# Performance work log

Hardware: AMD Instinct MI355X
Metric: run time of the kernel (lower is better)

Reference implementation:

```python
import jax, jax.numpy as jnp
import numpy as np

B, N, D = 8, 4096, 3
MAX_K = 16


def setup_inputs() -> dict:
    key = jax.random.key(0)
    k1, k2, k3 = jax.random.split(key, 3)
    x = jax.random.normal(k1, (B, N, D), dtype=jnp.float32)
    preds = jax.random.normal(k2, (B, N, D), dtype=jnp.float32)
    k_vector = jax.random.normal(k3, (MAX_K,), dtype=jnp.float32)  # learned param
    return {"x": x, "preds": preds, "k_vector": k_vector}


def _pairwise_dist(x):
    # Euclidean cdist via ||a||^2 + ||b||^2 - 2 a.b, avoiding a [B,N,N,D] tensor.
    sq = jnp.sum(x * x, axis=-1)                      # [B, N]
    inner = jnp.einsum('bnd,bmd->bnm', x, x)          # [B, N, N]
    d2 = sq[:, :, None] + sq[:, None, :] - 2.0 * inner
    return jnp.sqrt(jnp.maximum(d2, 0.0))             # [B, N, N]


def reference(x, preds, k_vector):
    # k = argmax(softmax(k_vector)) + 1 ; softmax is monotone so argmax suffices.
    # In the torch original .item() makes k a Python int (static w.r.t. the graph).
    k = int(np.asarray(jnp.argmax(k_vector))) + 1

    dist = _pairwise_dist(x)                          # [B, N, N]
    # torch.topk(..., largest=False): k smallest distances -> top_k of negated.
    _, idx = jax.lax.top_k(-dist, k)                  # idx: [B, N, k]

    # Gather predicted coords of the k nearest neighbors per point.
    b_idx = jnp.arange(preds.shape[0])[:, None, None]  # [B,1,1]
    knn_coords = preds[b_idx, idx]                     # [B, N, k, D]
    new_space = jnp.mean(knn_coords, axis=2)           # [B, N, D]
    return new_space
```

## Files before the change

kernel.cpp:

```cpp
#include <hip/hip_runtime.h>
#include <math.h>

typedef unsigned long long u64;
typedef unsigned int u32;

#define BB 8
#define NN 4096
#define MAXK 16
#define NSEG 4
#define BQ 64
#define CHUNK 512
#define BUFSLOTS 16

#define INSERT16(KEYV) do {                                                  \
    bool c_[MAXK];                                                           \
    _Pragma("unroll")                                                        \
    for (int s_ = 0; s_ < MAXK; ++s_) c_[s_] = (KEYV) < list[s_];            \
    _Pragma("unroll")                                                        \
    for (int s_ = MAXK - 1; s_ >= 1; --s_)                                   \
        list[s_] = c_[s_] ? (c_[s_ - 1] ? list[s_ - 1] : (KEYV)) : list[s_]; \
    list[0] = c_[0] ? (KEYV) : list[0];                                      \
    wkey = list[MAXK - 1];                                                   \
} while (0)

#define FLUSH() do {                                                         \
    _Pragma("unroll")                                                        \
    for (int i_ = 0; i_ < BUFSLOTS; ++i_) {                                  \
        const u64 fk_ = buf[i_][lane];                                       \
        if (i_ < cnt && fk_ < wkey) { INSERT16(fk_); }                       \
    }                                                                        \
    cnt = 0;                                                                 \
} while (0)

template <int SEGS, bool FUSED>
__global__ __launch_bounds__(BQ) void knn_scan(
    const float* __restrict__ x, const float* __restrict__ preds,
    const float* __restrict__ kvec, u64* __restrict__ ws,
    float* __restrict__ out)
{
    constexpr int SEGLEN = NN / SEGS;
    int bid = blockIdx.x;
    const int seg = bid % SEGS; bid /= SEGS;
    const int qg  = bid % (NN / BQ);
    const int b   = bid / (NN / BQ);
    const int lane = (int)threadIdx.x;
    const int qi = qg * BQ + lane;

    const float* xb = x + (size_t)b * NN * 3;
    const float qx = xb[qi * 3 + 0];
    const float qy = xb[qi * 3 + 1];
    const float qz = xb[qi * 3 + 2];
    const float qsq = __fadd_rn(__fadd_rn(__fmul_rn(qx, qx), __fmul_rn(qy, qy)),
                                __fmul_rn(qz, qz));

    __shared__ float4 cand[CHUNK];
    __shared__ u64 buf[BUFSLOTS][BQ];

    u64 list[MAXK];
#pragma unroll
    for (int s = 0; s < MAXK; ++s) list[s] = ~0ull;
    u64 wkey = ~0ull;
    int cnt = 0;

    const int jbase = seg * SEGLEN;
    for (int c0 = 0; c0 < SEGLEN; c0 += CHUNK) {
        __syncthreads();
        for (int t = lane; t < CHUNK; t += BQ) {
            const int j = jbase + c0 + t;
            const float cx = xb[j * 3 + 0];
            const float cy = xb[j * 3 + 1];
            const float cz = xb[j * 3 + 2];
            const float csq = __fadd_rn(
                __fadd_rn(__fmul_rn(cx, cx), __fmul_rn(cy, cy)),
                __fmul_rn(cz, cz));
            cand[t] = make_float4(cx, cy, cz, csq);
        }
        __syncthreads();

        for (int t = 0; t < CHUNK; t += 4) {
            if (__any((int)(cnt > BUFSLOTS - 4))) { FLUSH(); }
#pragma unroll
            for (int u = 0; u < 4; ++u) {
                const float4 c = cand[t + u];
                const float inner = __fadd_rn(
                    __fadd_rn(__fmul_rn(qx, c.x), __fmul_rn(qy, c.y)),
                    __fmul_rn(qz, c.z));
                float d2 = __fsub_rn(__fadd_rn(qsq, c.w), __fmul_rn(2.0f, inner));
                d2 = fmaxf(d2, 0.0f);
                const u64 key = ((u64)__float_as_uint(d2) << 32)
                              | (u32)(jbase + c0 + t + u);
                buf[cnt][lane] = key;
                cnt += (key < wkey) ? 1 : 0;
            }
        }
    }
    FLUSH();

    if (FUSED) {
        float bv = kvec[0]; int bi = 0;
#pragma unroll
        for (int i = 1; i < MAXK; ++i) { const float v = kvec[i]; if (v > bv) { bv = v; bi = i; } }
        const int k = bi + 1;
        const float* pb = preds + (size_t)b * NN * 3;
        float sx = 0.f, sy = 0.f, sz = 0.f;
#pragma unroll
        for (int s = 0; s < MAXK; ++s) {
            if (s < k) {
                const int j = (int)(u32)list[s];
                sx = __fadd_rn(sx, pb[j * 3 + 0]);
                sy = __fadd_rn(sy, pb[j * 3 + 1]);
                sz = __fadd_rn(sz, pb[j * 3 + 2]);
            }
        }
        const float fk = (float)k;
        float* ob = out + ((size_t)b * NN + qi) * 3;
        ob[0] = __fdiv_rn(sx, fk);
        ob[1] = __fdiv_rn(sy, fk);
        ob[2] = __fdiv_rn(sz, fk);
    } else {
        const size_t q = (size_t)b * NN + qi;
#pragma unroll
        for (int s = 0; s < MAXK; ++s)
            ws[(size_t)(seg * MAXK + s) * (BB * NN) + q] = list[s];
    }
}

__global__ __launch_bounds__(BQ) void knn_merge(
    const float* __restrict__ preds, const float* __restrict__ kvec,
    const u64* __restrict__ ws, float* __restrict__ out)
{
    const int q = blockIdx.x * BQ + (int)threadIdx.x;

    u64 list[MAXK];
#pragma unroll
    for (int s = 0; s < MAXK; ++s) list[s] = ~0ull;
    u64 wkey = ~0ull;

#pragma unroll 4
    for (int i = 0; i < NSEG * MAXK; ++i) {
        const u64 key = ws[(size_t)i * (BB * NN) + q];
        if (key < wkey) { INSERT16(key); }
    }

    float bv = kvec[0]; int bi = 0;
#pragma unroll
    for (int i = 1; i < MAXK; ++i) { const float v = kvec[i]; if (v > bv) { bv = v; bi = i; } }
    const int k = bi + 1;

    const int b = q / NN;
    const float* pb = preds + (size_t)b * NN * 3;
    float sx = 0.f, sy = 0.f, sz = 0.f;
#pragma unroll
    for (int s = 0; s < MAXK; ++s) {
        if (s < k) {
            const int j = (int)(u32)list[s];
            sx = __fadd_rn(sx, pb[j * 3 + 0]);
            sy = __fadd_rn(sy, pb[j * 3 + 1]);
            sz = __fadd_rn(sz, pb[j * 3 + 2]);
        }
    }
    const float fk = (float)k;
    out[(size_t)q * 3 + 0] = __fdiv_rn(sx, fk);
    out[(size_t)q * 3 + 1] = __fdiv_rn(sy, fk);
    out[(size_t)q * 3 + 2] = __fdiv_rn(sz, fk);
}

extern "C" void kernel_launch(void* const* d_in, const int* in_sizes, int n_in,
                              void* d_out, int out_size, void* d_ws, size_t ws_size,
                              hipStream_t stream) {
    (void)in_sizes; (void)n_in; (void)out_size;
    const float* x     = (const float*)d_in[0];
    const float* preds = (const float*)d_in[1];
    const float* kvec  = (const float*)d_in[2];
    float* out = (float*)d_out;

    const size_t ws_need = (size_t)NSEG * MAXK * BB * NN * sizeof(u64);
    if (ws_size >= ws_need) {
        u64* ws = (u64*)d_ws;
        knn_scan<NSEG, false><<<BB * (NN / BQ) * NSEG, BQ, 0, stream>>>(
            x, preds, kvec, ws, out);
        knn_merge<<<(BB * NN) / BQ, BQ, 0, stream>>>(preds, kvec, ws, out);
    } else {
        knn_scan<1, true><<<BB * (NN / BQ), BQ, 0, stream>>>(
            x, preds, kvec, nullptr, out);
    }
}
```

Measured before the change: 163.6 us.

## Use bitonic sort-merge flushes, precomputed float4 table, and 8-way segment split

```diff
diff --git a/kernel.cpp b/kernel.cpp
--- a/kernel.cpp
+++ b/kernel.cpp
@@ -7,148 +7,76 @@
 #define BB 8
 #define NN 4096
 #define MAXK 16
-#define NSEG 4
 #define BQ 64
-#define CHUNK 512
 #define BUFSLOTS 16
 
-#define INSERT16(KEYV) do {                                                  \
-    bool c_[MAXK];                                                           \
-    _Pragma("unroll")                                                        \
-    for (int s_ = 0; s_ < MAXK; ++s_) c_[s_] = (KEYV) < list[s_];            \
-    _Pragma("unroll")                                                        \
-    for (int s_ = MAXK - 1; s_ >= 1; --s_)                                   \
-        list[s_] = c_[s_] ? (c_[s_ - 1] ? list[s_ - 1] : (KEYV)) : list[s_]; \
-    list[0] = c_[0] ? (KEYV) : list[0];                                      \
-    wkey = list[MAXK - 1];                                                   \
-} while (0)
-
-#define FLUSH() do {                                                         \
-    _Pragma("unroll")                                                        \
-    for (int i_ = 0; i_ < BUFSLOTS; ++i_) {                                  \
-        const u64 fk_ = buf[i_][lane];                                       \
-        if (i_ < cnt && fk_ < wkey) { INSERT16(fk_); }                       \
-    }                                                                        \
-    cnt = 0;                                                                 \
-} while (0)
-
-template <int SEGS, bool FUSED>
-__global__ __launch_bounds__(BQ) void knn_scan(
-    const float* __restrict__ x, const float* __restrict__ preds,
-    const float* __restrict__ kvec, u64* __restrict__ ws,
-    float* __restrict__ out)
-{
-    constexpr int SEGLEN = NN / SEGS;
-    int bid = blockIdx.x;
-    const int seg = bid % SEGS; bid /= SEGS;
-    const int qg  = bid % (NN / BQ);
-    const int b   = bid / (NN / BQ);
-    const int lane = (int)threadIdx.x;
-    const int qi = qg * BQ + lane;
-
-    const float* xb = x + (size_t)b * NN * 3;
-    const float qx = xb[qi * 3 + 0];
-    const float qy = xb[qi * 3 + 1];
-    const float qz = xb[qi * 3 + 2];
-    const float qsq = __fadd_rn(__fadd_rn(__fmul_rn(qx, qx), __fmul_rn(qy, qy)),
-                                __fmul_rn(qz, qz));
-
-    __shared__ float4 cand[CHUNK];
-    __shared__ u64 buf[BUFSLOTS][BQ];
-
-    u64 list[MAXK];
-#pragma unroll
-    for (int s = 0; s < MAXK; ++s) list[s] = ~0ull;
-    u64 wkey = ~0ull;
-    int cnt = 0;
-
-    const int jbase = seg * SEGLEN;
-    for (int c0 = 0; c0 < SEGLEN; c0 += CHUNK) {
-        __syncthreads();
-        for (int t = lane; t < CHUNK; t += BQ) {
-            const int j = jbase + c0 + t;
-            const float cx = xb[j * 3 + 0];
-            const float cy = xb[j * 3 + 1];
-            const float cz = xb[j * 3 + 2];
-            const float csq = __fadd_rn(
-                __fadd_rn(__fmul_rn(cx, cx), __fmul_rn(cy, cy)),
-                __fmul_rn(cz, cz));
-            cand[t] = make_float4(cx, cy, cz, csq);
-        }
-        __syncthreads();
-
-        for (int t = 0; t < CHUNK; t += 4) {
-            if (__any((int)(cnt > BUFSLOTS - 4))) { FLUSH(); }
-#pragma unroll
-            for (int u = 0; u < 4; ++u) {
-                const float4 c = cand[t + u];
-                const float inner = __fadd_rn(
-                    __fadd_rn(__fmul_rn(qx, c.x), __fmul_rn(qy, c.y)),
-                    __fmul_rn(qz, c.z));
-                float d2 = __fsub_rn(__fadd_rn(qsq, c.w), __fmul_rn(2.0f, inner));
-                d2 = fmaxf(d2, 0.0f);
-                const u64 key = ((u64)__float_as_uint(d2) << 32)
-                              | (u32)(jbase + c0 + t + u);
-                buf[cnt][lane] = key;
-                cnt += (key < wkey) ? 1 : 0;
+
+__device__ __forceinline__ void bitonic16(u64 v[MAXK]) {
+#pragma unroll
+    for (int k = 2; k <= 16; k <<= 1) {
+#pragma unroll
+        for (int j = k >> 1; j > 0; j >>= 1) {
+#pragma unroll
+            for (int i = 0; i < 16; ++i) {
+                const int l = i ^ j;
+                if (l > i) {
+                    const u64 a = v[i], b = v[l];
+                    const bool up = ((i & k) == 0);
+                    const bool sw = up ? (a > b) : (a < b);
+                    v[i] = sw ? b : a;
+                    v[l] = sw ? a : b;
+                }
             }
         }
     }
-    FLUSH();
-
-    if (FUSED) {
-        float bv = kvec[0]; int bi = 0;
-#pragma unroll
-        for (int i = 1; i < MAXK; ++i) { const float v = kvec[i]; if (v > bv) { bv = v; bi = i; } }
-        const int k = bi + 1;
-        const float* pb = preds + (size_t)b * NN * 3;
-        float sx = 0.f, sy = 0.f, sz = 0.f;
-#pragma unroll
-        for (int s = 0; s < MAXK; ++s) {
-            if (s < k) {
-                const int j = (int)(u32)list[s];
-                sx = __fadd_rn(sx, pb[j * 3 + 0]);
-                sy = __fadd_rn(sy, pb[j * 3 + 1]);
-                sz = __fadd_rn(sz, pb[j * 3 + 2]);
+}
+
+__device__ __forceinline__ void merge16(u64 list[MAXK], const u64 br[MAXK]) {
+    u64 lo[MAXK];
+#pragma unroll
+    for (int i = 0; i < 16; ++i) {
+        const u64 a = list[i], b = br[15 - i];
+        lo[i] = a < b ? a : b;
+    }
+#pragma unroll
+    for (int j = 8; j > 0; j >>= 1) {
+#pragma unroll
+        for (int i = 0; i < 16; ++i) {
+            const int l = i ^ j;
+            if (l > i) {
+                const u64 a = lo[i], b = lo[l];
+                const bool sw = a > b;
+                lo[i] = sw ? b : a;
+                lo[l] = sw ? a : b;
             }
         }
-        const float fk = (float)k;
-        float* ob = out + ((size_t)b * NN + qi) * 3;
-        ob[0] = __fdiv_rn(sx, fk);
-        ob[1] = __fdiv_rn(sy, fk);
-        ob[2] = __fdiv_rn(sz, fk);
-    } else {
-        const size_t q = (size_t)b * NN + qi;
-#pragma unroll
-        for (int s = 0; s < MAXK; ++s)
-            ws[(size_t)(seg * MAXK + s) * (BB * NN) + q] = list[s];
-    }
-}
-
-__global__ __launch_bounds__(BQ) void knn_merge(
-    const float* __restrict__ preds, const float* __restrict__ kvec,
-    const u64* __restrict__ ws, float* __restrict__ out)
-{
-    const int q = blockIdx.x * BQ + (int)threadIdx.x;
-
-    u64 list[MAXK];
-#pragma unroll
-    for (int s = 0; s < MAXK; ++s) list[s] = ~0ull;
-    u64 wkey = ~0ull;
-
-#pragma unroll 4
-    for (int i = 0; i < NSEG * MAXK; ++i) {
-        const u64 key = ws[(size_t)i * (BB * NN) + q];
-        if (key < wkey) { INSERT16(key); }
-    }
-
+    }
+#pragma unroll
+    for (int i = 0; i < 16; ++i) list[i] = lo[i];
+}
+
+__device__ __forceinline__ void flush_buf(u64 list[MAXK], u64& wkey, int& cnt,
+                                          const u64 (*buf)[BQ], int lane) {
+    u64 br[MAXK];
+#pragma unroll
+    for (int i = 0; i < 16; ++i) {
+        const u64 v = buf[i][lane];
+        br[i] = (i < cnt) ? v : ~0ull;
+    }
+    bitonic16(br);
+    merge16(list, br);
+    wkey = list[15];
+    cnt = 0;
+}
+
+__device__ __forceinline__ void write_mean(const float* __restrict__ pb,
+                                           const float* __restrict__ kvec,
+                                           const u64 list[MAXK],
+                                           float* __restrict__ op) {
     float bv = kvec[0]; int bi = 0;
 #pragma unroll
     for (int i = 1; i < MAXK; ++i) { const float v = kvec[i]; if (v > bv) { bv = v; bi = i; } }
     const int k = bi + 1;
-
-    const int b = q / NN;
-    const float* pb = preds + (size_t)b * NN * 3;
     float sx = 0.f, sy = 0.f, sz = 0.f;
 #pragma unroll
     for (int s = 0; s < MAXK; ++s) {
@@ -160,9 +88,125 @@
         }
     }
     const float fk = (float)k;
-    out[(size_t)q * 3 + 0] = __fdiv_rn(sx, fk);
-    out[(size_t)q * 3 + 1] = __fdiv_rn(sy, fk);
-    out[(size_t)q * 3 + 2] = __fdiv_rn(sz, fk);
+    op[0] = __fdiv_rn(sx, fk);
+    op[1] = __fdiv_rn(sy, fk);
+    op[2] = __fdiv_rn(sz, fk);
+}
+
+__global__ __launch_bounds__(256) void knn_prep(const float* __restrict__ x,
+                                                float4* __restrict__ tab) {
+    const int i = blockIdx.x * 256 + (int)threadIdx.x;
+    const float cx = x[i * 3 + 0], cy = x[i * 3 + 1], cz = x[i * 3 + 2];
+    const float sq = __fadd_rn(__fadd_rn(__fmul_rn(cx, cx), __fmul_rn(cy, cy)),
+                               __fmul_rn(cz, cz));
+    tab[i] = make_float4(cx, cy, cz, sq);
+}
+
+template <int SEGS, bool TAB, bool FUSED>
+__global__ __launch_bounds__(BQ) void knn_scan(
+    const float* __restrict__ x, const float* __restrict__ preds,
+    const float* __restrict__ kvec, const float4* __restrict__ tab,
+    u64* __restrict__ wkeys, float* __restrict__ out)
+{
+    constexpr int SEGLEN = NN / SEGS;
+    int bid = blockIdx.x;
+    const int seg = bid % SEGS;
+    bid /= SEGS;
+    const int qg = bid % (NN / BQ);
+    const int b  = bid / (NN / BQ);
+    const int lane = (int)threadIdx.x;
+    const int qi = qg * BQ + lane;
+
+    const float* xb = x + (size_t)b * NN * 3;
+    const float4* tb = TAB ? (tab + (size_t)b * NN) : nullptr;
+
+    float qx, qy, qz, qsq;
+    if (TAB) {
+        const float4 qv = tb[qi];
+        qx = qv.x; qy = qv.y; qz = qv.z; qsq = qv.w;
+    } else {
+        qx = xb[qi * 3 + 0]; qy = xb[qi * 3 + 1]; qz = xb[qi * 3 + 2];
+        qsq = __fadd_rn(__fadd_rn(__fmul_rn(qx, qx), __fmul_rn(qy, qy)),
+                        __fmul_rn(qz, qz));
+    }
+
+    __shared__ u64 buf[BUFSLOTS][BQ];
+
+    u64 list[MAXK];
+#pragma unroll
+    for (int s = 0; s < MAXK; ++s) list[s] = ~0ull;
+    u64 wkey = ~0ull;
+    int cnt = 0;
+
+    const int jbase = seg * SEGLEN;
+#pragma unroll 1
+    for (int t = 0; t < SEGLEN; t += 4) {
+        if (__any((int)(cnt > BUFSLOTS - 4))) flush_buf(list, wkey, cnt, buf, lane);
+#pragma unroll
+        for (int u = 0; u < 4; ++u) {
+            const int j = jbase + t + u;
+            float cx, cy, cz, csq;
+            if (TAB) {
+                const float4 c = tb[j];
+                cx = c.x; cy = c.y; cz = c.z; csq = c.w;
+            } else {
+                cx = xb[j * 3 + 0]; cy = xb[j * 3 + 1]; cz = xb[j * 3 + 2];
+                csq = __fadd_rn(__fadd_rn(__fmul_rn(cx, cx), __fmul_rn(cy, cy)),
+                                __fmul_rn(cz, cz));
+            }
+            const float inner = __fadd_rn(
+                __fadd_rn(__fmul_rn(qx, cx), __fmul_rn(qy, cy)),
+                __fmul_rn(qz, cz));
+            float d2 = __fsub_rn(__fadd_rn(qsq, csq), __fmul_rn(2.0f, inner));
+            d2 = fmaxf(d2, 0.0f);
+            const u64 key = ((u64)__float_as_uint(d2) << 32) | (u32)j;
+            buf[cnt][lane] = key;
+            cnt += (key < wkey) ? 1 : 0;
+        }
+    }
+    flush_buf(list, wkey, cnt, buf, lane);
+
+    if (FUSED) {
+        write_mean(preds + (size_t)b * NN * 3, kvec, list,
+                   out + ((size_t)b * NN + qi) * 3);
+    } else {
+        const size_t q = (size_t)b * NN + qi;
+#pragma unroll
+        for (int s = 0; s < MAXK; ++s)
+            wkeys[(size_t)(seg * MAXK + s) * (BB * NN) + q] = list[s];
+    }
+}
+
+template <int SEGS>
+__global__ __launch_bounds__(BQ) void knn_merge(
+    const float* __restrict__ preds, const float* __restrict__ kvec,
+    const u64* __restrict__ wkeys, float* __restrict__ out)
+{
+    const int lane = (int)threadIdx.x;
+    const int q = blockIdx.x * BQ + lane;
+
+    __shared__ u64 buf[BUFSLOTS][BQ];
+
+    u64 list[MAXK];
+#pragma unroll
+    for (int s = 0; s < MAXK; ++s) list[s] = ~0ull;
+    u64 wkey = ~0ull;
+    int cnt = 0;
+
+#pragma unroll 1
+    for (int i = 0; i < SEGS * MAXK; i += 4) {
+        if (__any((int)(cnt > BUFSLOTS - 4))) flush_buf(list, wkey, cnt, buf, lane);
+#pragma unroll
+        for (int u = 0; u < 4; ++u) {
+            const u64 key = wkeys[(size_t)(i + u) * (BB * NN) + q];
+            buf[cnt][lane] = key;
+            cnt += (key < wkey) ? 1 : 0;
+        }
+    }
+    flush_buf(list, wkey, cnt, buf, lane);
+
+    const int b = q / NN;
+    write_mean(preds + (size_t)b * NN * 3, kvec, list, out + (size_t)q * 3);
 }
 
 extern "C" void kernel_launch(void* const* d_in, const int* in_sizes, int n_in,
@@ -174,14 +218,31 @@
     const float* kvec  = (const float*)d_in[2];
     float* out = (float*)d_out;
 
-    const size_t ws_need = (size_t)NSEG * MAXK * BB * NN * sizeof(u64);
-    if (ws_size >= ws_need) {
-        u64* ws = (u64*)d_ws;
-        knn_scan<NSEG, false><<<BB * (NN / BQ) * NSEG, BQ, 0, stream>>>(
-            x, preds, kvec, ws, out);
-        knn_merge<<<(BB * NN) / BQ, BQ, 0, stream>>>(preds, kvec, ws, out);
+    const size_t keys8 = 8ull * MAXK * BB * NN * sizeof(u64);
+    const size_t keys4 = 4ull * MAXK * BB * NN * sizeof(u64);
+    const size_t tabsz = (size_t)BB * NN * sizeof(float4);
+
+    if (ws_size >= keys8 + tabsz) {
+        u64* wkeys  = (u64*)d_ws;
+        float4* tab = (float4*)((char*)d_ws + keys8);
+        knn_prep<<<(BB * NN) / 256, 256, 0, stream>>>(x, tab);
+        knn_scan<8, true, false><<<BB * (NN / BQ) * 8, BQ, 0, stream>>>(
+            x, preds, kvec, tab, wkeys, out);
+        knn_merge<8><<<(BB * NN) / BQ, BQ, 0, stream>>>(preds, kvec, wkeys, out);
+    } else if (ws_size >= keys4 + tabsz) {
+        u64* wkeys  = (u64*)d_ws;
+        float4* tab = (float4*)((char*)d_ws + keys4);
+        knn_prep<<<(BB * NN) / 256, 256, 0, stream>>>(x, tab);
+        knn_scan<4, true, false><<<BB * (NN / BQ) * 4, BQ, 0, stream>>>(
+            x, preds, kvec, tab, wkeys, out);
+        knn_merge<4><<<(BB * NN) / BQ, BQ, 0, stream>>>(preds, kvec, wkeys, out);
+    } else if (ws_size >= keys4) {
+        u64* wkeys = (u64*)d_ws;
+        knn_scan<4, false, false><<<BB * (NN / BQ) * 4, BQ, 0, stream>>>(
+            x, preds, kvec, nullptr, wkeys, out);
+        knn_merge<4><<<(BB * NN) / BQ, BQ, 0, stream>>>(preds, kvec, wkeys, out);
     } else {
-        knn_scan<1, true><<<BB * (NN / BQ), BQ, 0, stream>>>(
-            x, preds, kvec, nullptr, out);
-    }
-}
+        knn_scan<1, false, true><<<BB * (NN / BQ), BQ, 0, stream>>>(
+            x, preds, kvec, nullptr, nullptr, out);
+    }
+}
```

Result: faster. 158.5 us (-3.2%).
